# Kernel optimization log

Hardware: AMD Instinct MI355X
Metric: run time of the kernel (lower is better)

Reference implementation:

```python
import jax, jax.numpy as jnp
import numpy as np

N_NODES = 100000
N_EDGES = 600000
D = 128
EPS = 1e-12  # F.normalize default eps


def _l2_normalize(v, axis=1):
    n = jnp.linalg.norm(v, axis=axis, keepdims=True)
    return v / jnp.maximum(n, EPS)


def setup_inputs() -> dict:
    key = jax.random.key(0)
    k1, k2, k3, k4, k5 = jax.random.split(key, 5)
    x = jax.random.normal(k1, (N_NODES, D), dtype=jnp.float32)
    edge_index = jax.random.randint(k2, (2, N_EDGES), 0, N_NODES, dtype=jnp.int64)
    edge_weight = jax.random.uniform(k3, (N_EDGES,), dtype=jnp.float32)
    W = jax.random.normal(k4, (D, 2 * D), dtype=jnp.float32) / np.sqrt(2 * D)
    b = jax.random.normal(k5, (D,), dtype=jnp.float32) * 0.01
    return {"x": x, "edge_index": edge_index, "edge_weight": edge_weight, "W": W, "b": b}


def reference(x, edge_index, edge_weight, W, b):
    src, dst = edge_index[0], edge_index[1]
    # message: x_j * edge_weight; aggregate: scatter-add at destination nodes
    msgs = x[src] * edge_weight[:, None]                       # [E, D]
    grads = jax.ops.segment_sum(msgs, dst, num_segments=N_NODES)  # [N, D]
    norm_grads = _l2_normalize(grads, axis=1)
    out = jnp.concatenate((x, norm_grads), axis=1)             # [N, 2D]
    out = out @ W.T + b                                        # Linear(2D -> D)
    return _l2_normalize(out, axis=1)
```

## Files before the change

kernel.cpp:

```cpp
#include <hip/hip_runtime.h>
#include <stdint.h>

typedef __attribute__((ext_vector_type(8))) short short8;
typedef __attribute__((ext_vector_type(4))) float f32x4;

__device__ __forceinline__ uint32_t f2bf1(float f) {
  union { float f; uint32_t u; } c; c.f = f;
  return (c.u + 0x7FFFu + ((c.u >> 16) & 1u)) >> 16;
}
__device__ __forceinline__ uint32_t pack2bf(float lo, float hi) {
  return f2bf1(lo) | (f2bf1(hi) << 16);
}
__device__ __forceinline__ float bflo(uint32_t u) {
  union { uint32_t u; float f; } c; c.u = u << 16; return c.f;
}
__device__ __forceinline__ float bfhi(uint32_t u) {
  union { uint32_t u; float f; } c; c.u = u & 0xFFFF0000u; return c.f;
}


__global__ void __launch_bounds__(256) zero_kernel(uint4* __restrict__ p, int n4) {
  int i = blockIdx.x * 256 + threadIdx.x;
  if (i < n4) p[i] = make_uint4(0u, 0u, 0u, 0u);
}

__global__ void __launch_bounds__(256) prep_kernel(
    const int* __restrict__ dst, uint32_t* __restrict__ deg,
    uint32_t* __restrict__ pos,
    const float* __restrict__ x, uint32_t* __restrict__ xbf,
    const float* __restrict__ W, uint32_t* __restrict__ wf,
    int E, int N, int eB, int xB) {
  int b = blockIdx.x;
  int ti = threadIdx.x;
  if (b < eB) {
    int e8 = (b * 256 + ti) * 8;
    if (e8 + 7 < E) {
      int4 da = *reinterpret_cast<const int4*>(dst + e8);
      int4 db = *reinterpret_cast<const int4*>(dst + e8 + 4);
      uint4 pa, pb;
      pa.x = atomicAdd(&deg[da.x], 1u);
      pa.y = atomicAdd(&deg[da.y], 1u);
      pa.z = atomicAdd(&deg[da.z], 1u);
      pa.w = atomicAdd(&deg[da.w], 1u);
      pb.x = atomicAdd(&deg[db.x], 1u);
      pb.y = atomicAdd(&deg[db.y], 1u);
      pb.z = atomicAdd(&deg[db.z], 1u);
      pb.w = atomicAdd(&deg[db.w], 1u);
      *reinterpret_cast<uint4*>(pos + e8) = pa;
      *reinterpret_cast<uint4*>(pos + e8 + 4) = pb;
    } else {
      for (int e = e8; e < E; ++e) pos[e] = atomicAdd(&deg[dst[e]], 1u);
    }
  } else if (b < eB + xB) {
    int n = (b - eB) * 32 + (ti >> 3);
    int c0 = ti & 7;
    if (n >= N) return;
    const float* xp0 = x + (size_t)n * 128 + c0 * 8;
    const float* xp1 = x + (size_t)n * 128 + (c0 + 8) * 8;
    float4 f0 = reinterpret_cast<const float4*>(xp0)[0];
    float4 f1 = reinterpret_cast<const float4*>(xp0)[1];
    float4 f2 = reinterpret_cast<const float4*>(xp1)[0];
    float4 f3 = reinterpret_cast<const float4*>(xp1)[1];
    uint4 pka, pkb;
    pka.x = pack2bf(f0.x, f0.y); pka.y = pack2bf(f0.z, f0.w);
    pka.z = pack2bf(f1.x, f1.y); pka.w = pack2bf(f1.z, f1.w);
    pkb.x = pack2bf(f2.x, f2.y); pkb.y = pack2bf(f2.z, f2.w);
    pkb.z = pack2bf(f3.x, f3.y); pkb.w = pack2bf(f3.z, f3.w);
    *reinterpret_cast<uint4*>(xbf + (size_t)n * 64 + c0 * 4) = pka;
    *reinterpret_cast<uint4*>(xbf + (size_t)n * 64 + (c0 + 8) * 4) = pkb;
  } else {
    int ch = (b - eB - xB) * 256 + ti;
    if (ch < 4096) {
      int nt = ch >> 9, ks = (ch >> 6) & 7, lane = ch & 63;
      int rw = nt * 16 + (lane & 15);
      const float* wp = W + (size_t)rw * 256 + ks * 32 + (lane >> 4) * 8;
      float4 f0 = reinterpret_cast<const float4*>(wp)[0];
      float4 f1 = reinterpret_cast<const float4*>(wp)[1];
      uint4 pk;
      pk.x = pack2bf(f0.x, f0.y); pk.y = pack2bf(f0.z, f0.w);
      pk.z = pack2bf(f1.x, f1.y); pk.w = pack2bf(f1.z, f1.w);
      reinterpret_cast<uint4*>(wf)[ch] = pk;
    }
  }
}

__global__ void __launch_bounds__(256) scan1_kernel(
    const uint32_t* __restrict__ deg, uint32_t* __restrict__ partial,
    uint32_t* __restrict__ bsum, int N) {
  __shared__ uint32_t sm[256];
  int t = threadIdx.x;
  int base = blockIdx.x * 1024 + t * 4;
  uint32_t d0 = 0, d1 = 0, d2 = 0, d3 = 0;
  if (base + 3 < N) {
    uint4 v = *reinterpret_cast<const uint4*>(deg + base);
    d0 = v.x; d1 = v.y; d2 = v.z; d3 = v.w;
  } else {
    if (base + 0 < N) d0 = deg[base + 0];
    if (base + 1 < N) d1 = deg[base + 1];
    if (base + 2 < N) d2 = deg[base + 2];
    if (base + 3 < N) d3 = deg[base + 3];
  }
  uint32_t s4 = d0 + d1 + d2 + d3;
  sm[t] = s4;
  uint32_t v = s4;
  __syncthreads();
  #pragma unroll
  for (int off = 1; off < 256; off <<= 1) {
    uint32_t u = (t >= off) ? sm[t - off] : 0u;
    __syncthreads();
    v += u;
    sm[t] = v;
    __syncthreads();
  }
  uint32_t ex = v - s4;
  if (base + 0 < N) partial[base + 0] = ex;
  if (base + 1 < N) partial[base + 1] = ex + d0;
  if (base + 2 < N) partial[base + 2] = ex + d0 + d1;
  if (base + 3 < N) partial[base + 3] = ex + d0 + d1 + d2;
  if (t == 255) bsum[blockIdx.x] = v;
}

__global__ void __launch_bounds__(1024) scan2_kernel(
    const uint32_t* __restrict__ bsum, uint32_t* __restrict__ boff, int nb) {
  __shared__ uint32_t sm[1024];
  int t = threadIdx.x;
  uint32_t s = (t < nb) ? bsum[t] : 0u;
  sm[t] = s;
  uint32_t v = s;
  __syncthreads();
  #pragma unroll
  for (int off = 1; off < 1024; off <<= 1) {
    uint32_t u = (t >= off) ? sm[t - off] : 0u;
    __syncthreads();
    v += u;
    sm[t] = v;
    __syncthreads();
  }
  if (t < nb) boff[t] = v - s;
}

__global__ void __launch_bounds__(256) fill_kernel(
    const int* __restrict__ src, const int* __restrict__ dst,
    const float* __restrict__ ew, const uint32_t* __restrict__ partial,
    const uint32_t* __restrict__ boff, const uint32_t* __restrict__ pos,
    uint2* __restrict__ pairs, int E) {
  int e = blockIdx.x * 256 + threadIdx.x;
  if (e < E) {
    int d = dst[e];
    union { float f; uint32_t u; } w; w.f = ew[e];
    pairs[partial[d] + boff[d >> 10] + pos[e]] = make_uint2((uint32_t)src[e], w.u);
  }
}

__global__ void __launch_bounds__(256) gather_kernel(
    const uint2* __restrict__ pairs, const uint32_t* __restrict__ partial,
    const uint32_t* __restrict__ boff, const uint32_t* __restrict__ deg,
    const uint32_t* __restrict__ xbf, uint32_t* __restrict__ ngf, int N) {
  int n = blockIdx.x * 4 + (threadIdx.x >> 6);
  if (n >= N) return;
  int lane = threadIdx.x & 63;
  int half = lane >> 5;
  int sl2 = lane & 31;
  uint32_t base = partial[n] + boff[n >> 10];
  int dn = (int)deg[n];

  uint2 mp = (lane < dn) ? pairs[base + lane] : make_uint2(0u, 0u);

  float a0 = 0.f, a1 = 0.f, a2 = 0.f, a3 = 0.f;
  int dcap = dn < 64 ? dn : 64;
  int iters = (dcap + 1) >> 1;
  int itp = (iters + 3) & ~3;
  for (int i = 0; i < itp; i += 4) {
    int k0 = (i + 0) * 2 + half;
    int k1 = (i + 1) * 2 + half;
    int k2 = (i + 2) * 2 + half;
    int k3 = (i + 3) * 2 + half;
    uint32_t s0 = (uint32_t)__shfl((int)mp.x, k0, 64);
    uint32_t s1 = (uint32_t)__shfl((int)mp.x, k1, 64);
    uint32_t s2 = (uint32_t)__shfl((int)mp.x, k2, 64);
    uint32_t s3 = (uint32_t)__shfl((int)mp.x, k3, 64);
    union { uint32_t u; float f; } w0, w1, w2, w3;
    w0.u = (uint32_t)__shfl((int)mp.y, k0, 64);
    w1.u = (uint32_t)__shfl((int)mp.y, k1, 64);
    w2.u = (uint32_t)__shfl((int)mp.y, k2, 64);
    w3.u = (uint32_t)__shfl((int)mp.y, k3, 64);
    uint2 v0 = reinterpret_cast<const uint2*>(xbf + (size_t)s0 * 64)[sl2];
    uint2 v1 = reinterpret_cast<const uint2*>(xbf + (size_t)s1 * 64)[sl2];
    uint2 v2 = reinterpret_cast<const uint2*>(xbf + (size_t)s2 * 64)[sl2];
    uint2 v3 = reinterpret_cast<const uint2*>(xbf + (size_t)s3 * 64)[sl2];
    a0 += w0.f * bflo(v0.x); a1 += w0.f * bfhi(v0.x);
    a2 += w0.f * bflo(v0.y); a3 += w0.f * bfhi(v0.y);
    a0 += w1.f * bflo(v1.x); a1 += w1.f * bfhi(v1.x);
    a2 += w1.f * bflo(v1.y); a3 += w1.f * bfhi(v1.y);
    a0 += w2.f * bflo(v2.x); a1 += w2.f * bfhi(v2.x);
    a2 += w2.f * bflo(v2.y); a3 += w2.f * bfhi(v2.y);
    a0 += w3.f * bflo(v3.x); a1 += w3.f * bfhi(v3.x);
    a2 += w3.f * bflo(v3.y); a3 += w3.f * bfhi(v3.y);
  }
  for (int k = 64 + half; k < dn; k += 2) {
    uint2 p = pairs[base + k];
    union { uint32_t u; float f; } w; w.u = p.y;
    uint2 v = reinterpret_cast<const uint2*>(xbf + (size_t)p.x * 64)[sl2];
    a0 += w.f * bflo(v.x);
    a1 += w.f * bfhi(v.x);
    a2 += w.f * bflo(v.y);
    a3 += w.f * bfhi(v.y);
  }

  a0 += __shfl_xor(a0, 32, 64);
  a1 += __shfl_xor(a1, 32, 64);
  a2 += __shfl_xor(a2, 32, 64);
  a3 += __shfl_xor(a3, 32, 64);

  float ss = a0 * a0 + a1 * a1 + a2 * a2 + a3 * a3;
  ss += __shfl_xor(ss, 1, 64);
  ss += __shfl_xor(ss, 2, 64);
  ss += __shfl_xor(ss, 4, 64);
  ss += __shfl_xor(ss, 8, 64);
  ss += __shfl_xor(ss, 16, 64);
  float scale = 1.0f / fmaxf(sqrtf(ss), 1e-12f);
  if (half == 0) {
    uint2 o;
    o.x = pack2bf(a0 * scale, a1 * scale);
    o.y = pack2bf(a2 * scale, a3 * scale);
    int t = n >> 4, rr = n & 15;
    uint32_t* dstp = ngf +
        ((size_t)(t * 4 + (sl2 >> 3)) * 64 + ((sl2 & 7) >> 1) * 16 + rr) * 4 +
        (sl2 & 1) * 2;
    *reinterpret_cast<uint2*>(dstp) = o;
  }
}

__global__ void __launch_bounds__(256) gemm_kernel(
    const uint32_t* __restrict__ xbf, const uint32_t* __restrict__ ngf,
    const uint32_t* __restrict__ wf, const float* __restrict__ bias,
    float* __restrict__ out, int N) {
  int wid = threadIdx.x >> 6;
  int lane = threadIdx.x & 63;
  int tile = blockIdx.x * 4 + wid;
  int node0 = tile * 32;
  if (node0 >= N) return;
  int r = lane & 15;
  int kg = lane >> 4;
  int t0 = tile * 2;

  short8 a0[8], a1[8];
  {
    const uint32_t* xr0 = xbf + (size_t)(node0 + r) * 64 + kg * 4;
    const uint32_t* xr1 = xr0 + 16 * 64;
    #pragma unroll
    for (int ks = 0; ks < 4; ++ks) {
      a0[ks] = *reinterpret_cast<const short8*>(xr0 + ks * 16);
      a1[ks] = *reinterpret_cast<const short8*>(xr1 + ks * 16);
    }
    #pragma unroll
    for (int ks = 0; ks < 4; ++ks) {
      a0[4 + ks] = *reinterpret_cast<const short8*>(
          ngf + ((size_t)(t0 * 4 + ks) * 64 + lane) * 4);
      a1[4 + ks] = *reinterpret_cast<const short8*>(
          ngf + ((size_t)((t0 + 1) * 4 + ks) * 64 + lane) * 4);
    }
  }

  f32x4 acc0[8], acc1[8];
  #pragma unroll
  for (int nt = 0; nt < 8; ++nt) {
    acc0[nt] = (f32x4){0.f, 0.f, 0.f, 0.f};
    acc1[nt] = (f32x4){0.f, 0.f, 0.f, 0.f};
  }

  #pragma unroll
  for (int nt = 0; nt < 8; ++nt) {
    #pragma unroll
    for (int ks = 0; ks < 8; ++ks) {
      short8 bfrag = *reinterpret_cast<const short8*>(
          wf + ((size_t)(nt * 8 + ks) * 64 + lane) * 4);
      acc0[nt] = __builtin_amdgcn_mfma_f32_16x16x32_bf16(a0[ks], bfrag, acc0[nt], 0, 0, 0);
      acc1[nt] = __builtin_amdgcn_mfma_f32_16x16x32_bf16(a1[ks], bfrag, acc1[nt], 0, 0, 0);
    }
  }

  float bv[8];
  #pragma unroll
  for (int nt = 0; nt < 8; ++nt) bv[nt] = bias[nt * 16 + r];

  #pragma unroll
  for (int st = 0; st < 2; ++st) {
    f32x4* acc = st ? acc1 : acc0;
    int nodeb = node0 + st * 16;
    #pragma unroll
    for (int reg = 0; reg < 4; ++reg) {
      float ss = 0.f;
      #pragma unroll
      for (int nt = 0; nt < 8; ++nt) {
        float v = acc[nt][reg] + bv[nt];
        acc[nt][reg] = v;
        ss += v * v;
      }
      ss += __shfl_xor(ss, 1, 64);
      ss += __shfl_xor(ss, 2, 64);
      ss += __shfl_xor(ss, 4, 64);
      ss += __shfl_xor(ss, 8, 64);
      float scale = 1.0f / fmaxf(sqrtf(ss), 1e-12f);
      float* orow = out + (size_t)(nodeb + kg * 4 + reg) * 128;
      #pragma unroll
      for (int nt = 0; nt < 8; ++nt)
        orow[nt * 16 + r] = acc[nt][reg] * scale;
    }
  }
}

extern "C" void kernel_launch(void* const* d_in, const int* in_sizes, int n_in,
                              void* d_out, int out_size, void* d_ws, size_t ws_size,
                              hipStream_t stream) {
  const float* x    = (const float*)d_in[0];
  const int*   ei   = (const int*)d_in[1];
  const float* ew   = (const float*)d_in[2];
  const float* W    = (const float*)d_in[3];
  const float* bias = (const float*)d_in[4];
  float* out = (float*)d_out;

  int N = in_sizes[0] / 128;
  int E = in_sizes[1] / 2;
  const int* src = ei;
  const int* dst = ei + E;
  int nb = (N + 1023) / 1024;

  uint32_t* ngf = (uint32_t*)d_ws;
  uint32_t* wf  = ngf + (size_t)N * 64;
  uint32_t* xbf = wf + 16384;

  uint32_t* o       = (uint32_t*)d_out;
  uint32_t* deg     = o;
  uint32_t* partial = o + N;
  uint32_t* bsum    = o + 2 * (size_t)N;
  uint32_t* boff    = o + 2 * (size_t)N + 1024;
  uint2*    pairs   = (uint2*)(o + 2 * (size_t)N + 2048);
  uint32_t* pos     = o + 2 * (size_t)N + 2048 + 2 * (size_t)E;

  int eB = (E + 2047) / 2048;
  int xB = (N + 31) / 32;
  int n4 = (N + 3) / 4;
  zero_kernel<<<(n4 + 255) / 256, 256, 0, stream>>>((uint4*)deg, n4);
  prep_kernel<<<eB + xB + 16, 256, 0, stream>>>(
      dst, deg, pos, x, xbf, W, wf, E, N, eB, xB);
  scan1_kernel<<<nb, 256, 0, stream>>>(deg, partial, bsum, N);
  scan2_kernel<<<1, 1024, 0, stream>>>(bsum, boff, nb);
  fill_kernel<<<(E + 255) / 256, 256, 0, stream>>>(src, dst, ew, partial, boff,
                                                   pos, pairs, E);
  gather_kernel<<<(N + 3) / 4, 256, 0, stream>>>(pairs, partial, boff, deg,
                                                 xbf, ngf, N);
  int ntiles32 = (N + 31) / 32;
  gemm_kernel<<<(ntiles32 + 3) / 4, 256, 0, stream>>>(xbf, ngf, wf, bias, out, N);
}
```

Before: 125.2 us.

## Fuse neighbor gather and MFMA linear layer into one kernel via LDS

Merges the gather/normalize kernel and the GEMM kernel into one kernel. Each wave now aggregates 32 nodes one after another and writes the normalized bf16 rows into shared memory, then runs the MFMA linear layer and output normalization directly from that staging. This removes the global round trip of the intermediate normalized-gradient buffer and one kernel launch. In exchange, the latency-bound gather is serialized within each wave, which sharply reduces the number of independent waves and outstanding memory requests. Scratch buffers are moved from the output buffer into the workspace, and row-bound guards are added.

```diff
diff --git a/kernel.cpp b/kernel.cpp
--- a/kernel.cpp
+++ b/kernel.cpp
@@ -152,113 +152,108 @@
   }
 }
 
-__global__ void __launch_bounds__(256) gather_kernel(
+__global__ void __launch_bounds__(256) gg_kernel(
     const uint2* __restrict__ pairs, const uint32_t* __restrict__ partial,
     const uint32_t* __restrict__ boff, const uint32_t* __restrict__ deg,
-    const uint32_t* __restrict__ xbf, uint32_t* __restrict__ ngf, int N) {
-  int n = blockIdx.x * 4 + (threadIdx.x >> 6);
-  if (n >= N) return;
+    const uint32_t* __restrict__ xbf, const uint32_t* __restrict__ wf,
+    const float* __restrict__ bias, float* __restrict__ out, int N) {
+  __shared__ uint32_t ng[128][68];
+  int wid = threadIdx.x >> 6;
   int lane = threadIdx.x & 63;
+  int node0 = blockIdx.x * 128 + wid * 32;
+  if (node0 >= N) return;
   int half = lane >> 5;
   int sl2 = lane & 31;
-  uint32_t base = partial[n] + boff[n >> 10];
-  int dn = (int)deg[n];
-
-  uint2 mp = (lane < dn) ? pairs[base + lane] : make_uint2(0u, 0u);
-
-  float a0 = 0.f, a1 = 0.f, a2 = 0.f, a3 = 0.f;
-  int dcap = dn < 64 ? dn : 64;
-  int iters = (dcap + 1) >> 1;
-  int itp = (iters + 3) & ~3;
-  for (int i = 0; i < itp; i += 4) {
-    int k0 = (i + 0) * 2 + half;
-    int k1 = (i + 1) * 2 + half;
-    int k2 = (i + 2) * 2 + half;
-    int k3 = (i + 3) * 2 + half;
-    uint32_t s0 = (uint32_t)__shfl((int)mp.x, k0, 64);
-    uint32_t s1 = (uint32_t)__shfl((int)mp.x, k1, 64);
-    uint32_t s2 = (uint32_t)__shfl((int)mp.x, k2, 64);
-    uint32_t s3 = (uint32_t)__shfl((int)mp.x, k3, 64);
-    union { uint32_t u; float f; } w0, w1, w2, w3;
-    w0.u = (uint32_t)__shfl((int)mp.y, k0, 64);
-    w1.u = (uint32_t)__shfl((int)mp.y, k1, 64);
-    w2.u = (uint32_t)__shfl((int)mp.y, k2, 64);
-    w3.u = (uint32_t)__shfl((int)mp.y, k3, 64);
-    uint2 v0 = reinterpret_cast<const uint2*>(xbf + (size_t)s0 * 64)[sl2];
-    uint2 v1 = reinterpret_cast<const uint2*>(xbf + (size_t)s1 * 64)[sl2];
-    uint2 v2 = reinterpret_cast<const uint2*>(xbf + (size_t)s2 * 64)[sl2];
-    uint2 v3 = reinterpret_cast<const uint2*>(xbf + (size_t)s3 * 64)[sl2];
-    a0 += w0.f * bflo(v0.x); a1 += w0.f * bfhi(v0.x);
-    a2 += w0.f * bflo(v0.y); a3 += w0.f * bfhi(v0.y);
-    a0 += w1.f * bflo(v1.x); a1 += w1.f * bfhi(v1.x);
-    a2 += w1.f * bflo(v1.y); a3 += w1.f * bfhi(v1.y);
-    a0 += w2.f * bflo(v2.x); a1 += w2.f * bfhi(v2.x);
-    a2 += w2.f * bflo(v2.y); a3 += w2.f * bfhi(v2.y);
-    a0 += w3.f * bflo(v3.x); a1 += w3.f * bfhi(v3.x);
-    a2 += w3.f * bflo(v3.y); a3 += w3.f * bfhi(v3.y);
-  }
-  for (int k = 64 + half; k < dn; k += 2) {
-    uint2 p = pairs[base + k];
-    union { uint32_t u; float f; } w; w.u = p.y;
-    uint2 v = reinterpret_cast<const uint2*>(xbf + (size_t)p.x * 64)[sl2];
-    a0 += w.f * bflo(v.x);
-    a1 += w.f * bfhi(v.x);
-    a2 += w.f * bflo(v.y);
-    a3 += w.f * bfhi(v.y);
-  }
-
-  a0 += __shfl_xor(a0, 32, 64);
-  a1 += __shfl_xor(a1, 32, 64);
-  a2 += __shfl_xor(a2, 32, 64);
-  a3 += __shfl_xor(a3, 32, 64);
-
-  float ss = a0 * a0 + a1 * a1 + a2 * a2 + a3 * a3;
-  ss += __shfl_xor(ss, 1, 64);
-  ss += __shfl_xor(ss, 2, 64);
-  ss += __shfl_xor(ss, 4, 64);
-  ss += __shfl_xor(ss, 8, 64);
-  ss += __shfl_xor(ss, 16, 64);
-  float scale = 1.0f / fmaxf(sqrtf(ss), 1e-12f);
-  if (half == 0) {
-    uint2 o;
-    o.x = pack2bf(a0 * scale, a1 * scale);
-    o.y = pack2bf(a2 * scale, a3 * scale);
-    int t = n >> 4, rr = n & 15;
-    uint32_t* dstp = ngf +
-        ((size_t)(t * 4 + (sl2 >> 3)) * 64 + ((sl2 & 7) >> 1) * 16 + rr) * 4 +
-        (sl2 & 1) * 2;
-    *reinterpret_cast<uint2*>(dstp) = o;
-  }
-}
-
-__global__ void __launch_bounds__(256) gemm_kernel(
-    const uint32_t* __restrict__ xbf, const uint32_t* __restrict__ ngf,
-    const uint32_t* __restrict__ wf, const float* __restrict__ bias,
-    float* __restrict__ out, int N) {
-  int wid = threadIdx.x >> 6;
-  int lane = threadIdx.x & 63;
-  int tile = blockIdx.x * 4 + wid;
-  int node0 = tile * 32;
-  if (node0 >= N) return;
+  int lbase = wid * 32;
+
+  for (int j = 0; j < 32; ++j) {
+    int n = node0 + j;
+    if (n >= N) break;
+    uint32_t base = partial[n] + boff[n >> 10];
+    int dn = (int)deg[n];
+    uint2 mp = (lane < dn) ? pairs[base + lane] : make_uint2(0u, 0u);
+
+    float a0 = 0.f, a1 = 0.f, a2 = 0.f, a3 = 0.f;
+    int dcap = dn < 64 ? dn : 64;
+    int iters = (dcap + 1) >> 1;
+    int itp = (iters + 3) & ~3;
+    for (int i = 0; i < itp; i += 4) {
+      int k0 = (i + 0) * 2 + half;
+      int k1 = (i + 1) * 2 + half;
+      int k2 = (i + 2) * 2 + half;
+      int k3 = (i + 3) * 2 + half;
+      uint32_t s0 = (uint32_t)__shfl((int)mp.x, k0, 64);
+      uint32_t s1 = (uint32_t)__shfl((int)mp.x, k1, 64);
+      uint32_t s2 = (uint32_t)__shfl((int)mp.x, k2, 64);
+      uint32_t s3 = (uint32_t)__shfl((int)mp.x, k3, 64);
+      union { uint32_t u; float f; } w0, w1, w2, w3;
+      w0.u = (uint32_t)__shfl((int)mp.y, k0, 64);
+      w1.u = (uint32_t)__shfl((int)mp.y, k1, 64);
+      w2.u = (uint32_t)__shfl((int)mp.y, k2, 64);
+      w3.u = (uint32_t)__shfl((int)mp.y, k3, 64);
+      uint2 v0 = reinterpret_cast<const uint2*>(xbf + (size_t)s0 * 64)[sl2];
+      uint2 v1 = reinterpret_cast<const uint2*>(xbf + (size_t)s1 * 64)[sl2];
+      uint2 v2 = reinterpret_cast<const uint2*>(xbf + (size_t)s2 * 64)[sl2];
+      uint2 v3 = reinterpret_cast<const uint2*>(xbf + (size_t)s3 * 64)[sl2];
+      a0 += w0.f * bflo(v0.x); a1 += w0.f * bfhi(v0.x);
+      a2 += w0.f * bflo(v0.y); a3 += w0.f * bfhi(v0.y);
+      a0 += w1.f * bflo(v1.x); a1 += w1.f * bfhi(v1.x);
+      a2 += w1.f * bflo(v1.y); a3 += w1.f * bfhi(v1.y);
+      a0 += w2.f * bflo(v2.x); a1 += w2.f * bfhi(v2.x);
+      a2 += w2.f * bflo(v2.y); a3 += w2.f * bfhi(v2.y);
+      a0 += w3.f * bflo(v3.x); a1 += w3.f * bfhi(v3.x);
+      a2 += w3.f * bflo(v3.y); a3 += w3.f * bfhi(v3.y);
+    }
+    for (int k = 64 + half; k < dn; k += 2) {
+      uint2 p = pairs[base + k];
+      union { uint32_t u; float f; } w; w.u = p.y;
+      uint2 v = reinterpret_cast<const uint2*>(xbf + (size_t)p.x * 64)[sl2];
+      a0 += w.f * bflo(v.x);
+      a1 += w.f * bfhi(v.x);
+      a2 += w.f * bflo(v.y);
+      a3 += w.f * bfhi(v.y);
+    }
+
+    a0 += __shfl_xor(a0, 32, 64);
+    a1 += __shfl_xor(a1, 32, 64);
+    a2 += __shfl_xor(a2, 32, 64);
+    a3 += __shfl_xor(a3, 32, 64);
+
+    float ss = a0 * a0 + a1 * a1 + a2 * a2 + a3 * a3;
+    ss += __shfl_xor(ss, 1, 64);
+    ss += __shfl_xor(ss, 2, 64);
+    ss += __shfl_xor(ss, 4, 64);
+    ss += __shfl_xor(ss, 8, 64);
+    ss += __shfl_xor(ss, 16, 64);
+    float scale = 1.0f / fmaxf(sqrtf(ss), 1e-12f);
+    if (half == 0) {
+      uint2 o;
+      o.x = pack2bf(a0 * scale, a1 * scale);
+      o.y = pack2bf(a2 * scale, a3 * scale);
+      *reinterpret_cast<uint2*>(&ng[lbase + j][2 * sl2]) = o;
+    }
+  }
+
   int r = lane & 15;
   int kg = lane >> 4;
-  int t0 = tile * 2;
-
-  short8 a0[8], a1[8];
+
+  short8 a0f[8], a1f[8];
   {
-    const uint32_t* xr0 = xbf + (size_t)(node0 + r) * 64 + kg * 4;
-    const uint32_t* xr1 = xr0 + 16 * 64;
+    int rw0 = node0 + r;       if (rw0 > N - 1) rw0 = N - 1;
+    int rw1 = node0 + 16 + r;  if (rw1 > N - 1) rw1 = N - 1;
+    const uint32_t* xr0 = xbf + (size_t)rw0 * 64 + kg * 4;
+    const uint32_t* xr1 = xbf + (size_t)rw1 * 64 + kg * 4;
     #pragma unroll
     for (int ks = 0; ks < 4; ++ks) {
-      a0[ks] = *reinterpret_cast<const short8*>(xr0 + ks * 16);
-      a1[ks] = *reinterpret_cast<const short8*>(xr1 + ks * 16);
+      a0f[ks] = *reinterpret_cast<const short8*>(xr0 + ks * 16);
+      a1f[ks] = *reinterpret_cast<const short8*>(xr1 + ks * 16);
     }
     #pragma unroll
     for (int ks = 0; ks < 4; ++ks) {
-      a0[4 + ks] = *reinterpret_cast<const short8*>(
-          ngf + ((size_t)(t0 * 4 + ks) * 64 + lane) * 4);
-      a1[4 + ks] = *reinterpret_cast<const short8*>(
-          ngf + ((size_t)((t0 + 1) * 4 + ks) * 64 + lane) * 4);
+      a0f[4 + ks] = *reinterpret_cast<const short8*>(
+          &ng[lbase + r][ks * 16 + kg * 4]);
+      a1f[4 + ks] = *reinterpret_cast<const short8*>(
+          &ng[lbase + 16 + r][ks * 16 + kg * 4]);
     }
   }
 
@@ -275,8 +270,8 @@
     for (int ks = 0; ks < 8; ++ks) {
       short8 bfrag = *reinterpret_cast<const short8*>(
           wf + ((size_t)(nt * 8 + ks) * 64 + lane) * 4);
-      acc0[nt] = __builtin_amdgcn_mfma_f32_16x16x32_bf16(a0[ks], bfrag, acc0[nt], 0, 0, 0);
-      acc1[nt] = __builtin_amdgcn_mfma_f32_16x16x32_bf16(a1[ks], bfrag, acc1[nt], 0, 0, 0);
+      acc0[nt] = __builtin_amdgcn_mfma_f32_16x16x32_bf16(a0f[ks], bfrag, acc0[nt], 0, 0, 0);
+      acc1[nt] = __builtin_amdgcn_mfma_f32_16x16x32_bf16(a1f[ks], bfrag, acc1[nt], 0, 0, 0);
     }
   }
 
@@ -302,10 +297,13 @@
       ss += __shfl_xor(ss, 4, 64);
       ss += __shfl_xor(ss, 8, 64);
       float scale = 1.0f / fmaxf(sqrtf(ss), 1e-12f);
-      float* orow = out + (size_t)(nodeb + kg * 4 + reg) * 128;
-      #pragma unroll
-      for (int nt = 0; nt < 8; ++nt)
-        orow[nt * 16 + r] = acc[nt][reg] * scale;
+      int row = nodeb + kg * 4 + reg;
+      if (row < N) {
+        float* orow = out + (size_t)row * 128;
+        #pragma unroll
+        for (int nt = 0; nt < 8; ++nt)
+          orow[nt * 16 + r] = acc[nt][reg] * scale;
+      }
     }
   }
 }
@@ -326,17 +324,14 @@
   const int* dst = ei + E;
   int nb = (N + 1023) / 1024;
 
-  uint32_t* ngf = (uint32_t*)d_ws;
-  uint32_t* wf  = ngf + (size_t)N * 64;
-  uint32_t* xbf = wf + 16384;
-
-  uint32_t* o       = (uint32_t*)d_out;
-  uint32_t* deg     = o;
-  uint32_t* partial = o + N;
-  uint32_t* bsum    = o + 2 * (size_t)N;
-  uint32_t* boff    = o + 2 * (size_t)N + 1024;
-  uint2*    pairs   = (uint2*)(o + 2 * (size_t)N + 2048);
-  uint32_t* pos     = o + 2 * (size_t)N + 2048 + 2 * (size_t)E;
+  uint32_t* wf      = (uint32_t*)d_ws;
+  uint32_t* xbf     = wf + 16384;
+  uint32_t* deg     = xbf + (size_t)N * 64;
+  uint32_t* partial = deg + N;
+  uint32_t* bsum    = partial + N;
+  uint32_t* boff    = bsum + 1024;
+  uint2*    pairs   = (uint2*)(boff + 1024);
+  uint32_t* pos     = (uint32_t*)(pairs + E);
 
   int eB = (E + 2047) / 2048;
   int xB = (N + 31) / 32;
@@ -348,8 +343,7 @@
   scan2_kernel<<<1, 1024, 0, stream>>>(bsum, boff, nb);
   fill_kernel<<<(E + 255) / 256, 256, 0, stream>>>(src, dst, ew, partial, boff,
                                                    pos, pairs, E);
-  gather_kernel<<<(N + 3) / 4, 256, 0, stream>>>(pairs, partial, boff, deg,
-                                                 xbf, ngf, N);
-  int ntiles32 = (N + 31) / 32;
-  gemm_kernel<<<(ntiles32 + 3) / 4, 256, 0, stream>>>(xbf, ngf, wf, bias, out, N);
-}
+  int gB = (N + 127) / 128;
+  gg_kernel<<<gB, 256, 0, stream>>>(pairs, partial, boff, deg, xbf, wf,
+                                    bias, out, N);
+}
```

Measured after the change: 183.0 us. 46.2% more time.
